# Kernel optimization log

Measured on AMD Instinct MI355X. Metric: run time of the kernel, lower is better.

Reference implementation:

```python
import jax, jax.numpy as jnp
import numpy as np
import math

N_EMBD = 1024
N_HEAD = 16
HEAD_DIM = N_EMBD // N_HEAD


def setup_inputs() -> dict:
    key = jax.random.key(0)
    ks = jax.random.split(key, 9)
    B, T, E = 4, 2048, N_EMBD
    s = 0.02
    inp = {
        "x": jax.random.normal(ks[0], (B, T, E), dtype=jnp.float32),
        "Wq": jax.random.normal(ks[1], (E, E), dtype=jnp.float32) * s,
        "bq": jnp.zeros((E,), dtype=jnp.float32),
        "Wk": jax.random.normal(ks[2], (E, E), dtype=jnp.float32) * s,
        "bk": jnp.zeros((E,), dtype=jnp.float32),
        "Wv": jax.random.normal(ks[3], (E, E), dtype=jnp.float32) * s,
        "bv": jnp.zeros((E,), dtype=jnp.float32),
        "Wo": jax.random.normal(ks[4], (E, E), dtype=jnp.float32) * s,
        "bo": jnp.zeros((E,), dtype=jnp.float32),
    }
    return inp


def reference(x, Wq, bq, Wk, bk, Wv, bv, Wo, bo):
    B, T, E = x.shape
    H, D = N_HEAD, HEAD_DIM
    # Linear projections (torch Linear: y = x @ W.T + b)
    Q = (x @ Wq.T + bq).reshape(B, T, H, D).transpose(0, 2, 1, 3)  # [B,H,T,D]
    K = (x @ Wk.T + bk).reshape(B, T, H, D).transpose(0, 2, 1, 3)
    V = (x @ Wv.T + bv).reshape(B, T, H, D).transpose(0, 2, 1, 3)
    scale = 1.0 / math.sqrt(D)
    scores = jnp.einsum("bhqd,bhkd->bhqk", Q, K) * scale  # [B,H,T,T]
    causal = jnp.tril(jnp.ones((T, T), dtype=bool))
    scores = jnp.where(causal, scores, jnp.float32(-jnp.inf))
    probs = jax.nn.softmax(scores, axis=-1)
    out = jnp.einsum("bhqk,bhkd->bhqd", probs, V)  # [B,H,T,D]
    out = out.transpose(0, 2, 1, 3).reshape(B, T, E)
    return out @ Wo.T + bo
```

## Files before the change

### kernel.cpp

```cpp
#include <hip/hip_runtime.h>
#include <math.h>


typedef __bf16 bf16x8 __attribute__((ext_vector_type(8)));
typedef float f32x4 __attribute__((ext_vector_type(4)));
typedef unsigned int u32x4 __attribute__((ext_vector_type(4)));
typedef unsigned int uint;
typedef unsigned short ushort;

#define B_ 4
#define T_ 2048
#define E_ 1024
#define H_ 16
#define D_ 64
#define BT_ (B_ * T_)

__device__ __forceinline__ f32x4 mfma16(bf16x8 a, bf16x8 b, f32x4 c) {
  return __builtin_amdgcn_mfma_f32_16x16x32_bf16(a, b, c, 0, 0, 0);
}

__device__ __forceinline__ void gl_lds16(void* lds, const void* g) {
  __builtin_amdgcn_global_load_lds(
      (__attribute__((address_space(1))) unsigned int*)g,
      (__attribute__((address_space(3))) unsigned int*)lds, 16, 0, 0);
}

__device__ __forceinline__ uint pkbf(float a, float b) {
  ushort ux = __builtin_bit_cast(ushort, (__bf16)a);
  ushort uy = __builtin_bit_cast(ushort, (__bf16)b);
  return (uint)ux | ((uint)uy << 16);
}

__global__ __launch_bounds__(256) void cvt_bf16(const float* __restrict__ in,
                                                __bf16* __restrict__ out, int n) {
  int i = (blockIdx.x * 256 + threadIdx.x) * 8;
  if (i >= n) return;
  float4 a = *(const float4*)&in[i];
  float4 b = *(const float4*)&in[i + 4];
  bf16x8 o;
  o[0] = (__bf16)a.x; o[1] = (__bf16)a.y; o[2] = (__bf16)a.z; o[3] = (__bf16)a.w;
  o[4] = (__bf16)b.x; o[5] = (__bf16)b.y; o[6] = (__bf16)b.z; o[7] = (__bf16)b.w;
  *(bf16x8*)&out[i] = o;
}

__global__ __launch_bounds__(256) void cvt_w4(const float* __restrict__ w0,
                                              const float* __restrict__ w1,
                                              const float* __restrict__ w2,
                                              const float* __restrict__ w3,
                                              __bf16* __restrict__ o0,
                                              __bf16* __restrict__ o1,
                                              __bf16* __restrict__ o2,
                                              __bf16* __restrict__ o3) {
  const float* in;
  __bf16* out;
  switch (blockIdx.y) {
    case 0: in = w0; out = o0; break;
    case 1: in = w1; out = o1; break;
    case 2: in = w2; out = o2; break;
    default: in = w3; out = o3; break;
  }
  int i = (blockIdx.x * 256 + threadIdx.x) * 8;
  float4 a = *(const float4*)&in[i];
  float4 b = *(const float4*)&in[i + 4];
  bf16x8 o;
  o[0] = (__bf16)a.x; o[1] = (__bf16)a.y; o[2] = (__bf16)a.z; o[3] = (__bf16)a.w;
  o[4] = (__bf16)b.x; o[5] = (__bf16)b.y; o[6] = (__bf16)b.z; o[7] = (__bf16)b.w;
  *(bf16x8*)&out[i] = o;
}

template <int MODE>
__global__ __launch_bounds__(256) void gemm_nt(const __bf16* __restrict__ A,
                                               const __bf16* __restrict__ Bm,
                                               const float* __restrict__ bias,
                                               void* __restrict__ out,
                                               int M, int N, int K) {
  __shared__ __bf16 sA[128 * 32];
  __shared__ __bf16 sB[128 * 32];
  const int tid = threadIdx.x;
  const int lane = tid & 63;
  const int wv = tid >> 6;
  const int wr = (wv >> 1) << 6;
  const int wc = (wv & 1) << 6;
  const int fr = lane & 15;
  const int fo = (lane >> 4) << 3;
  const int g = lane >> 4;
  const int m0 = blockIdx.y * 128;
  const int n0 = blockIdx.x * 128;

  f32x4 acc[4][4] = {};

  const __bf16* aRow = A + (size_t)(m0 + (tid >> 2)) * K + ((tid & 3) << 3);
  const __bf16* bRow = Bm + (size_t)(n0 + (tid >> 2)) * K + ((tid & 3) << 3);

  for (int kt = 0; kt < K; kt += 32) {
    gl_lds16(&sA[(size_t)tid * 8], aRow + kt);
    gl_lds16(&sA[(size_t)(256 + tid) * 8], aRow + (size_t)64 * K + kt);
    gl_lds16(&sB[(size_t)tid * 8], bRow + kt);
    gl_lds16(&sB[(size_t)(256 + tid) * 8], bRow + (size_t)64 * K + kt);
    __syncthreads();
    bf16x8 af[4], bq[4];
#pragma unroll
    for (int i = 0; i < 4; i++) af[i] = *(const bf16x8*)&sA[(wr + i * 16 + fr) * 32 + fo];
#pragma unroll
    for (int i = 0; i < 4; i++) bq[i] = *(const bf16x8*)&sB[(wc + i * 16 + fr) * 32 + fo];
#pragma unroll
    for (int i = 0; i < 4; i++)
#pragma unroll
      for (int j = 0; j < 4; j++) acc[i][j] = mfma16(af[i], bq[j], acc[i][j]);
    __syncthreads();
  }

#pragma unroll
  for (int i = 0; i < 4; i++) {
#pragma unroll
    for (int j = 0; j < 4; j++) {
#pragma unroll
      for (int r = 0; r < 4; r++) {
        const int m = m0 + wr + i * 16 + g * 4 + r;
        const int n = n0 + wc + j * 16 + fr;
        float v = acc[i][j][r] + bias[n];
        ((float*)out)[(size_t)m * N + n] = v;
      }
    }
  }
}

__global__ __launch_bounds__(256) void gemm_qkv(const __bf16* __restrict__ xb,
                                                const __bf16* __restrict__ Wq,
                                                const __bf16* __restrict__ Wk,
                                                const __bf16* __restrict__ Wv,
                                                const float* __restrict__ bq,
                                                const float* __restrict__ bk,
                                                const float* __restrict__ bv,
                                                __bf16* __restrict__ Qb,
                                                __bf16* __restrict__ Kb,
                                                __bf16* __restrict__ Vtb) {
  __shared__ __bf16 sA[128 * 32];
  __shared__ __bf16 sB[128 * 32];
  const int z = blockIdx.z;
  const __bf16* A;
  const __bf16* Bm;
  const float* bias;
  int m0, n0;
  if (z == 0) {
    A = xb; Bm = Wq; bias = bq;
    m0 = blockIdx.y * 128; n0 = blockIdx.x * 128;
  } else if (z == 1) {
    A = xb; Bm = Wk; bias = bk;
    m0 = blockIdx.y * 128; n0 = blockIdx.x * 128;
  } else {
    A = Wv; Bm = xb; bias = bv;
    m0 = blockIdx.x * 128; n0 = blockIdx.y * 128;
  }
  const int K = E_;
  const int tid = threadIdx.x;
  const int lane = tid & 63;
  const int wv = tid >> 6;
  const int wr = (wv >> 1) << 6;
  const int wc = (wv & 1) << 6;
  const int fr = lane & 15;
  const int fo = (lane >> 4) << 3;
  const int g = lane >> 4;

  f32x4 acc[4][4] = {};

  const __bf16* aRow = A + (size_t)(m0 + (tid >> 2)) * K + ((tid & 3) << 3);
  const __bf16* bRow = Bm + (size_t)(n0 + (tid >> 2)) * K + ((tid & 3) << 3);

  for (int kt = 0; kt < K; kt += 32) {
    gl_lds16(&sA[(size_t)tid * 8], aRow + kt);
    gl_lds16(&sA[(size_t)(256 + tid) * 8], aRow + (size_t)64 * K + kt);
    gl_lds16(&sB[(size_t)tid * 8], bRow + kt);
    gl_lds16(&sB[(size_t)(256 + tid) * 8], bRow + (size_t)64 * K + kt);
    __syncthreads();
    bf16x8 af[4], bq4[4];
#pragma unroll
    for (int i = 0; i < 4; i++) af[i] = *(const bf16x8*)&sA[(wr + i * 16 + fr) * 32 + fo];
#pragma unroll
    for (int i = 0; i < 4; i++) bq4[i] = *(const bf16x8*)&sB[(wc + i * 16 + fr) * 32 + fo];
#pragma unroll
    for (int i = 0; i < 4; i++)
#pragma unroll
      for (int j = 0; j < 4; j++) acc[i][j] = mfma16(af[i], bq4[j], acc[i][j]);
    __syncthreads();
  }

#pragma unroll
  for (int i = 0; i < 4; i++) {
#pragma unroll
    for (int j = 0; j < 4; j++) {
#pragma unroll
      for (int r = 0; r < 4; r++) {
        const int m = m0 + wr + i * 16 + g * 4 + r;
        const int n = n0 + wc + j * 16 + fr;
        float v = acc[i][j][r];
        if (z == 2) {
          v += bias[m];
          const int b = n >> 11, t = n & (T_ - 1);
          const int h = m >> 6, d = m & 63;
          Vtb[(((size_t)b * H_ + h) * D_ + d) * T_ + t] = (__bf16)v;
        } else {
          v += bias[n];
          const int b = m >> 11, t = m & (T_ - 1);
          const int h = n >> 6, d = n & 63;
          __bf16* out = (z == 0) ? Qb : Kb;
          out[(((size_t)b * H_ + h) * T_ + t) * D_ + d] = (__bf16)v;
        }
      }
    }
  }
}

__global__ __launch_bounds__(512) void attn_fwd(const __bf16* __restrict__ Q,
                                                const __bf16* __restrict__ Kg,
                                                const __bf16* __restrict__ Vt,
                                                __bf16* __restrict__ O) {
  __shared__ __bf16 sK[2][64 * 64];
  __shared__ __bf16 sV[2][64 * 64];
  const int tid = threadIdx.x;
  const int lane = tid & 63;
  const int wv = tid >> 6;
  const int fr = lane & 15;
  const int g = lane >> 4;
  const int k = blockIdx.x;
  const int bh = (k & 7) | ((k >> 6) << 3);
  const int pr = (k >> 3) & 7;
  const __bf16* Qp = Q + (size_t)bh * T_ * D_;
  const __bf16* Kp = Kg + (size_t)bh * T_ * D_;
  const __bf16* Vp = Vt + (size_t)bh * D_ * T_;
  const float SCL = 0.125f * 1.44269504088896f;
  const int addrA = (fr + 32 * (g & 1)) * 4;
  const int swz = fr & 7;
  const int b = bh >> 4, h = bh & 15;

  auto stage = [&](int buf, int kv0) {
    const int row = tid >> 3, ch = tid & 7;
    gl_lds16(&sK[buf][tid * 8],
             Kp + (size_t)(kv0 + row) * D_ + ((ch ^ (row & 7)) << 3));
    gl_lds16(&sV[buf][tid * 8],
             Vp + (size_t)row * T_ + kv0 + ((ch ^ (row & 7)) << 3));
  };

#pragma unroll 1
  for (int pass = 0; pass < 2; ++pass) {
    const int s = pass ? 15 - pr : pr;
    const int qw = s * 128 + wv * 16;
    const int ntile = 2 * s + 2;

    bf16x8 qf[2];
#pragma unroll
    for (int kc = 0; kc < 2; kc++)
      qf[kc] = *(const bf16x8*)&Qp[(size_t)(qw + fr) * D_ + kc * 32 + g * 8];

    f32x4 acc[4] = {};
    float mrun = -INFINITY;
    float lrun = 0.f;

    stage(0, 0);
    __syncthreads();
    int cur = 0;

#pragma unroll 1
    for (int kt = 0; kt < ntile; ++kt) {
      const int kv0 = kt << 6;
      if (kt + 1 < ntile) stage(cur ^ 1, (kt + 1) << 6);

      if (kv0 <= qw + 15) {
        f32x4 st[4] = {};
        __builtin_amdgcn_s_setprio(1);
#pragma unroll
        for (int kvf = 0; kvf < 4; ++kvf) {
          const int row = kvf * 16 + fr;
          bf16x8 kf0 = *(const bf16x8*)&sK[cur][row * 64 + ((g ^ swz) << 3)];
          bf16x8 kf1 = *(const bf16x8*)&sK[cur][row * 64 + (((g + 4) ^ swz) << 3)];
          st[kvf] = mfma16(kf0, qf[0], st[kvf]);
          st[kvf] = mfma16(kf1, qf[1], st[kvf]);
        }
        __builtin_amdgcn_s_setprio(0);

        if (kv0 + 63 > qw) {
#pragma unroll
          for (int kvf = 0; kvf < 4; ++kvf)
#pragma unroll
            for (int r = 0; r < 4; ++r)
              if (kv0 + kvf * 16 + g * 4 + r > qw + fr) st[kvf][r] = -INFINITY;
        }

        float rm[4];
#pragma unroll
        for (int kvf = 0; kvf < 4; ++kvf)
          rm[kvf] = fmaxf(fmaxf(st[kvf][0], st[kvf][1]),
                          fmaxf(st[kvf][2], st[kvf][3]));
        float rmax = fmaxf(fmaxf(rm[0], rm[1]), fmaxf(rm[2], rm[3])) * SCL;

        if (!__all(rmax - mrun <= 8.f)) {
          float rfull = fmaxf(rmax, __shfl_xor(rmax, 16, 64));
          rfull = fmaxf(rfull, __shfl_xor(rfull, 32, 64));
          const float mn = fmaxf(mrun, rfull);
          const float corr = exp2f(mrun - mn);
          mrun = mn;
          lrun *= corr;
          float cg[4];
#pragma unroll
          for (int r = 0; r < 4; ++r) cg[r] = __shfl(corr, g * 4 + r, 64);
#pragma unroll
          for (int nd = 0; nd < 4; ++nd)
#pragma unroll
            for (int r = 0; r < 4; ++r) acc[nd][r] *= cg[r];
        }

        float p[4][4];
        float ls = 0.f;
#pragma unroll
        for (int kvf = 0; kvf < 4; ++kvf)
#pragma unroll
          for (int r = 0; r < 4; ++r) {
            p[kvf][r] = exp2f(fmaf(st[kvf][r], SCL, -mrun));
            ls += p[kvf][r];
          }
        lrun += ls;

        uint w[4][2];
#pragma unroll
        for (int kvf = 0; kvf < 4; ++kvf) {
          w[kvf][0] = pkbf(p[kvf][0], p[kvf][1]);
          w[kvf][1] = pkbf(p[kvf][2], p[kvf][3]);
        }
        uint W[2][4];
#pragma unroll
        for (int kc = 0; kc < 2; ++kc)
#pragma unroll
          for (int m = 0; m < 4; ++m) {
            const int a = addrA + (m >> 1) * 64;
            int t0 = __builtin_amdgcn_ds_bpermute(a, (int)w[2 * kc][m & 1]);
            int t1 = __builtin_amdgcn_ds_bpermute(a, (int)w[2 * kc + 1][m & 1]);
            W[kc][m] = (uint)((g >> 1) ? t1 : t0);
          }

        __builtin_amdgcn_s_setprio(1);
#pragma unroll
        for (int kc = 0; kc < 2; ++kc) {
          u32x4 t;
          t[0] = W[kc][0]; t[1] = W[kc][1]; t[2] = W[kc][2]; t[3] = W[kc][3];
          bf16x8 pa = __builtin_bit_cast(bf16x8, t);
#pragma unroll
          for (int nd = 0; nd < 4; ++nd) {
            const int row = nd * 16 + fr;
            bf16x8 vf =
                *(const bf16x8*)&sV[cur][row * 64 + (((4 * kc + g) ^ swz) << 3)];
            acc[nd] = mfma16(pa, vf, acc[nd]);
          }
        }
        __builtin_amdgcn_s_setprio(0);
      }

      __syncthreads();
      cur ^= 1;
    }

    lrun += __shfl_xor(lrun, 16, 64);
    lrun += __shfl_xor(lrun, 32, 64);
    float linv[4];
#pragma unroll
    for (int r = 0; r < 4; ++r) linv[r] = 1.f / __shfl(lrun, g * 4 + r, 64);
#pragma unroll
    for (int nd = 0; nd < 4; ++nd)
#pragma unroll
      for (int r = 0; r < 4; ++r) {
        const int t = qw + g * 4 + r;
        O[(((size_t)b * T_ + t) * H_ + h) * D_ + nd * 16 + fr] =
            (__bf16)(acc[nd][r] * linv[r]);
      }
  }
}

extern "C" void kernel_launch(void* const* d_in, const int* in_sizes, int n_in,
                              void* d_out, int out_size, void* d_ws, size_t ws_size,
                              hipStream_t stream) {
  const float* x  = (const float*)d_in[0];
  const float* Wq = (const float*)d_in[1];
  const float* bq = (const float*)d_in[2];
  const float* Wk = (const float*)d_in[3];
  const float* bk = (const float*)d_in[4];
  const float* Wv = (const float*)d_in[5];
  const float* bv = (const float*)d_in[6];
  const float* Wo = (const float*)d_in[7];
  const float* bo = (const float*)d_in[8];

  char* w = (char*)d_ws;
  __bf16* xb  = (__bf16*)w; w += (size_t)BT_ * E_ * 2;
  __bf16* Wqb = (__bf16*)w; w += (size_t)E_ * E_ * 2;
  __bf16* Wkb = (__bf16*)w; w += (size_t)E_ * E_ * 2;
  __bf16* Wvb = (__bf16*)w; w += (size_t)E_ * E_ * 2;
  __bf16* Wob = (__bf16*)w; w += (size_t)E_ * E_ * 2;
  __bf16* Qb  = (__bf16*)w; w += (size_t)BT_ * E_ * 2;
  __bf16* Kb  = (__bf16*)w; w += (size_t)BT_ * E_ * 2;
  __bf16* Vtb = (__bf16*)w; w += (size_t)BT_ * E_ * 2;
  __bf16* Ob  = (__bf16*)w; w += (size_t)BT_ * E_ * 2;

  cvt_bf16<<<(BT_ * E_) / 2048, 256, 0, stream>>>(x, xb, BT_ * E_);
  cvt_w4<<<dim3((E_ * E_) / 2048, 4), 256, 0, stream>>>(Wq, Wk, Wv, Wo,
                                                        Wqb, Wkb, Wvb, Wob);

  gemm_qkv<<<dim3(E_ / 128, BT_ / 128, 3), 256, 0, stream>>>(
      xb, Wqb, Wkb, Wvb, bq, bk, bv, Qb, Kb, Vtb);

  attn_fwd<<<512, 512, 0, stream>>>(Qb, Kb, Vtb, Ob);

  gemm_nt<2><<<dim3(E_ / 128, BT_ / 128), 256, 0, stream>>>(Ob, Wob, bo, d_out, BT_, E_, E_);
}
```

Measured before the change: 207.9 us.

## Use 128-wide KV tiles in attention, fold softmax scale into Q, swap grid order

The attention kernel now stages 128-key K/V tiles instead of 64, with a wider XOR swizzle for V. This halves the number of tile iterations and barriers per query block, at the cost of doubled LDS and more registers for the score and probability arrays. The softmax scale times log2(e) is folded into Q in the QKV GEMM epilogue, which removes a multiply per score. The QKV and output GEMM grids are swapped so blockIdx.x walks the M dimension, which changes the block launch order and L2 reuse.

```diff
diff --git a/kernel.cpp b/kernel.cpp
--- a/kernel.cpp
+++ b/kernel.cpp
@@ -30,6 +30,8 @@
   ushort uy = __builtin_bit_cast(ushort, (__bf16)b);
   return (uint)ux | ((uint)uy << 16);
 }
+
+#define QSCL 0.18033688011112f
 
 __global__ __launch_bounds__(256) void cvt_bf16(const float* __restrict__ in,
                                                 __bf16* __restrict__ out, int n) {
@@ -68,12 +70,11 @@
   *(bf16x8*)&out[i] = o;
 }
 
-template <int MODE>
-__global__ __launch_bounds__(256) void gemm_nt(const __bf16* __restrict__ A,
-                                               const __bf16* __restrict__ Bm,
-                                               const float* __restrict__ bias,
-                                               void* __restrict__ out,
-                                               int M, int N, int K) {
+__global__ __launch_bounds__(256) void gemm_out(const __bf16* __restrict__ A,
+                                                const __bf16* __restrict__ Bm,
+                                                const float* __restrict__ bias,
+                                                float* __restrict__ out,
+                                                int M, int N, int K) {
   __shared__ __bf16 sA[128 * 32];
   __shared__ __bf16 sB[128 * 32];
   const int tid = threadIdx.x;
@@ -84,8 +85,8 @@
   const int fr = lane & 15;
   const int fo = (lane >> 4) << 3;
   const int g = lane >> 4;
-  const int m0 = blockIdx.y * 128;
-  const int n0 = blockIdx.x * 128;
+  const int m0 = blockIdx.x * 128;
+  const int n0 = blockIdx.y * 128;
 
   f32x4 acc[4][4] = {};
 
@@ -118,8 +119,7 @@
       for (int r = 0; r < 4; r++) {
         const int m = m0 + wr + i * 16 + g * 4 + r;
         const int n = n0 + wc + j * 16 + fr;
-        float v = acc[i][j][r] + bias[n];
-        ((float*)out)[(size_t)m * N + n] = v;
+        out[(size_t)m * N + n] = acc[i][j][r] + bias[n];
       }
     }
   }
@@ -144,13 +144,13 @@
   int m0, n0;
   if (z == 0) {
     A = xb; Bm = Wq; bias = bq;
-    m0 = blockIdx.y * 128; n0 = blockIdx.x * 128;
+    m0 = blockIdx.x * 128; n0 = blockIdx.y * 128;
   } else if (z == 1) {
     A = xb; Bm = Wk; bias = bk;
-    m0 = blockIdx.y * 128; n0 = blockIdx.x * 128;
+    m0 = blockIdx.x * 128; n0 = blockIdx.y * 128;
   } else {
     A = Wv; Bm = xb; bias = bv;
-    m0 = blockIdx.x * 128; n0 = blockIdx.y * 128;
+    m0 = blockIdx.y * 128; n0 = blockIdx.x * 128;
   }
   const int K = E_;
   const int tid = threadIdx.x;
@@ -201,6 +201,7 @@
           Vtb[(((size_t)b * H_ + h) * D_ + d) * T_ + t] = (__bf16)v;
         } else {
           v += bias[n];
+          if (z == 0) v *= QSCL;
           const int b = m >> 11, t = m & (T_ - 1);
           const int h = n >> 6, d = n & 63;
           __bf16* out = (z == 0) ? Qb : Kb;
@@ -215,8 +216,8 @@
                                                 const __bf16* __restrict__ Kg,
                                                 const __bf16* __restrict__ Vt,
                                                 __bf16* __restrict__ O) {
-  __shared__ __bf16 sK[2][64 * 64];
-  __shared__ __bf16 sV[2][64 * 64];
+  __shared__ __bf16 sK[2][128 * 64];
+  __shared__ __bf16 sV[2][64 * 128];
   const int tid = threadIdx.x;
   const int lane = tid & 63;
   const int wv = tid >> 6;
@@ -228,24 +229,27 @@
   const __bf16* Qp = Q + (size_t)bh * T_ * D_;
   const __bf16* Kp = Kg + (size_t)bh * T_ * D_;
   const __bf16* Vp = Vt + (size_t)bh * D_ * T_;
-  const float SCL = 0.125f * 1.44269504088896f;
   const int addrA = (fr + 32 * (g & 1)) * 4;
-  const int swz = fr & 7;
   const int b = bh >> 4, h = bh & 15;
 
   auto stage = [&](int buf, int kv0) {
-    const int row = tid >> 3, ch = tid & 7;
-    gl_lds16(&sK[buf][tid * 8],
-             Kp + (size_t)(kv0 + row) * D_ + ((ch ^ (row & 7)) << 3));
-    gl_lds16(&sV[buf][tid * 8],
-             Vp + (size_t)row * T_ + kv0 + ((ch ^ (row & 7)) << 3));
+#pragma unroll
+    for (int rr = 0; rr < 2; ++rr) {
+      const int idx = rr * 512 + tid;
+      const int krow = idx >> 3, kch = idx & 7;
+      gl_lds16(&sK[buf][idx * 8],
+               Kp + (size_t)(kv0 + krow) * D_ + ((kch ^ (krow & 7)) << 3));
+      const int vrow = idx >> 4, vch = idx & 15;
+      gl_lds16(&sV[buf][idx * 8],
+               Vp + (size_t)vrow * T_ + kv0 + ((vch ^ (vrow & 15)) << 3));
+    }
   };
 
 #pragma unroll 1
   for (int pass = 0; pass < 2; ++pass) {
     const int s = pass ? 15 - pr : pr;
     const int qw = s * 128 + wv * 16;
-    const int ntile = 2 * s + 2;
+    const int ntile = s + 1;
 
     bf16x8 qf[2];
 #pragma unroll
@@ -262,97 +266,97 @@
 
 #pragma unroll 1
     for (int kt = 0; kt < ntile; ++kt) {
-      const int kv0 = kt << 6;
-      if (kt + 1 < ntile) stage(cur ^ 1, (kt + 1) << 6);
-
-      if (kv0 <= qw + 15) {
-        f32x4 st[4] = {};
-        __builtin_amdgcn_s_setprio(1);
-#pragma unroll
-        for (int kvf = 0; kvf < 4; ++kvf) {
-          const int row = kvf * 16 + fr;
-          bf16x8 kf0 = *(const bf16x8*)&sK[cur][row * 64 + ((g ^ swz) << 3)];
-          bf16x8 kf1 = *(const bf16x8*)&sK[cur][row * 64 + (((g + 4) ^ swz) << 3)];
-          st[kvf] = mfma16(kf0, qf[0], st[kvf]);
-          st[kvf] = mfma16(kf1, qf[1], st[kvf]);
+      const int kv0 = kt << 7;
+      if (kt + 1 < ntile) stage(cur ^ 1, (kt + 1) << 7);
+
+      f32x4 st[8] = {};
+      __builtin_amdgcn_s_setprio(1);
+#pragma unroll
+      for (int kvf = 0; kvf < 8; ++kvf) {
+        const int row = kvf * 16 + fr;
+        bf16x8 kf0 = *(const bf16x8*)&sK[cur][row * 64 + ((g ^ (fr & 7)) << 3)];
+        bf16x8 kf1 =
+            *(const bf16x8*)&sK[cur][row * 64 + (((g + 4) ^ (fr & 7)) << 3)];
+        st[kvf] = mfma16(kf0, qf[0], st[kvf]);
+        st[kvf] = mfma16(kf1, qf[1], st[kvf]);
+      }
+      __builtin_amdgcn_s_setprio(0);
+
+      if (kv0 + 127 > qw) {
+#pragma unroll
+        for (int kvf = 0; kvf < 8; ++kvf)
+#pragma unroll
+          for (int r = 0; r < 4; ++r)
+            if (kv0 + kvf * 16 + g * 4 + r > qw + fr) st[kvf][r] = -INFINITY;
+      }
+
+      float rm[8];
+#pragma unroll
+      for (int kvf = 0; kvf < 8; ++kvf)
+        rm[kvf] =
+            fmaxf(fmaxf(st[kvf][0], st[kvf][1]), fmaxf(st[kvf][2], st[kvf][3]));
+      float rmax = fmaxf(fmaxf(fmaxf(rm[0], rm[1]), fmaxf(rm[2], rm[3])),
+                         fmaxf(fmaxf(rm[4], rm[5]), fmaxf(rm[6], rm[7])));
+
+      if (!__all(rmax - mrun <= 8.f)) {
+        float rfull = fmaxf(rmax, __shfl_xor(rmax, 16, 64));
+        rfull = fmaxf(rfull, __shfl_xor(rfull, 32, 64));
+        const float mn = fmaxf(mrun, rfull);
+        const float corr = exp2f(mrun - mn);
+        mrun = mn;
+        lrun *= corr;
+        float cg[4];
+#pragma unroll
+        for (int r = 0; r < 4; ++r) cg[r] = __shfl(corr, g * 4 + r, 64);
+#pragma unroll
+        for (int nd = 0; nd < 4; ++nd)
+#pragma unroll
+          for (int r = 0; r < 4; ++r) acc[nd][r] *= cg[r];
+      }
+
+      float p[8][4];
+      float ls = 0.f;
+#pragma unroll
+      for (int kvf = 0; kvf < 8; ++kvf)
+#pragma unroll
+        for (int r = 0; r < 4; ++r) {
+          p[kvf][r] = exp2f(st[kvf][r] - mrun);
+          ls += p[kvf][r];
         }
-        __builtin_amdgcn_s_setprio(0);
-
-        if (kv0 + 63 > qw) {
-#pragma unroll
-          for (int kvf = 0; kvf < 4; ++kvf)
-#pragma unroll
-            for (int r = 0; r < 4; ++r)
-              if (kv0 + kvf * 16 + g * 4 + r > qw + fr) st[kvf][r] = -INFINITY;
+      lrun += ls;
+
+      uint w[8][2];
+#pragma unroll
+      for (int kvf = 0; kvf < 8; ++kvf) {
+        w[kvf][0] = pkbf(p[kvf][0], p[kvf][1]);
+        w[kvf][1] = pkbf(p[kvf][2], p[kvf][3]);
+      }
+      uint W[4][4];
+#pragma unroll
+      for (int kc = 0; kc < 4; ++kc)
+#pragma unroll
+        for (int m = 0; m < 4; ++m) {
+          const int a = addrA + (m >> 1) * 64;
+          int t0 = __builtin_amdgcn_ds_bpermute(a, (int)w[2 * kc][m & 1]);
+          int t1 = __builtin_amdgcn_ds_bpermute(a, (int)w[2 * kc + 1][m & 1]);
+          W[kc][m] = (uint)((g >> 1) ? t1 : t0);
         }
 
-        float rm[4];
-#pragma unroll
-        for (int kvf = 0; kvf < 4; ++kvf)
-          rm[kvf] = fmaxf(fmaxf(st[kvf][0], st[kvf][1]),
-                          fmaxf(st[kvf][2], st[kvf][3]));
-        float rmax = fmaxf(fmaxf(rm[0], rm[1]), fmaxf(rm[2], rm[3])) * SCL;
-
-        if (!__all(rmax - mrun <= 8.f)) {
-          float rfull = fmaxf(rmax, __shfl_xor(rmax, 16, 64));
-          rfull = fmaxf(rfull, __shfl_xor(rfull, 32, 64));
-          const float mn = fmaxf(mrun, rfull);
-          const float corr = exp2f(mrun - mn);
-          mrun = mn;
-          lrun *= corr;
-          float cg[4];
-#pragma unroll
-          for (int r = 0; r < 4; ++r) cg[r] = __shfl(corr, g * 4 + r, 64);
-#pragma unroll
-          for (int nd = 0; nd < 4; ++nd)
-#pragma unroll
-            for (int r = 0; r < 4; ++r) acc[nd][r] *= cg[r];
+      __builtin_amdgcn_s_setprio(1);
+#pragma unroll
+      for (int kc = 0; kc < 4; ++kc) {
+        u32x4 t;
+        t[0] = W[kc][0]; t[1] = W[kc][1]; t[2] = W[kc][2]; t[3] = W[kc][3];
+        bf16x8 pa = __builtin_bit_cast(bf16x8, t);
+#pragma unroll
+        for (int nd = 0; nd < 4; ++nd) {
+          const int row = nd * 16 + fr;
+          bf16x8 vf =
+              *(const bf16x8*)&sV[cur][row * 128 + (((4 * kc + g) ^ fr) << 3)];
+          acc[nd] = mfma16(pa, vf, acc[nd]);
         }
-
-        float p[4][4];
-        float ls = 0.f;
-#pragma unroll
-        for (int kvf = 0; kvf < 4; ++kvf)
-#pragma unroll
-          for (int r = 0; r < 4; ++r) {
-            p[kvf][r] = exp2f(fmaf(st[kvf][r], SCL, -mrun));
-            ls += p[kvf][r];
-          }
-        lrun += ls;
-
-        uint w[4][2];
-#pragma unroll
-        for (int kvf = 0; kvf < 4; ++kvf) {
-          w[kvf][0] = pkbf(p[kvf][0], p[kvf][1]);
-          w[kvf][1] = pkbf(p[kvf][2], p[kvf][3]);
-        }
-        uint W[2][4];
-#pragma unroll
-        for (int kc = 0; kc < 2; ++kc)
-#pragma unroll
-          for (int m = 0; m < 4; ++m) {
-            const int a = addrA + (m >> 1) * 64;
-            int t0 = __builtin_amdgcn_ds_bpermute(a, (int)w[2 * kc][m & 1]);
-            int t1 = __builtin_amdgcn_ds_bpermute(a, (int)w[2 * kc + 1][m & 1]);
-            W[kc][m] = (uint)((g >> 1) ? t1 : t0);
-          }
-
-        __builtin_amdgcn_s_setprio(1);
-#pragma unroll
-        for (int kc = 0; kc < 2; ++kc) {
-          u32x4 t;
-          t[0] = W[kc][0]; t[1] = W[kc][1]; t[2] = W[kc][2]; t[3] = W[kc][3];
-          bf16x8 pa = __builtin_bit_cast(bf16x8, t);
-#pragma unroll
-          for (int nd = 0; nd < 4; ++nd) {
-            const int row = nd * 16 + fr;
-            bf16x8 vf =
-                *(const bf16x8*)&sV[cur][row * 64 + (((4 * kc + g) ^ swz) << 3)];
-            acc[nd] = mfma16(pa, vf, acc[nd]);
-          }
-        }
-        __builtin_amdgcn_s_setprio(0);
-      }
+      }
+      __builtin_amdgcn_s_setprio(0);
 
       __syncthreads();
       cur ^= 1;
@@ -402,10 +406,11 @@
   cvt_w4<<<dim3((E_ * E_) / 2048, 4), 256, 0, stream>>>(Wq, Wk, Wv, Wo,
                                                         Wqb, Wkb, Wvb, Wob);
 
-  gemm_qkv<<<dim3(E_ / 128, BT_ / 128, 3), 256, 0, stream>>>(
+  gemm_qkv<<<dim3(BT_ / 128, E_ / 128, 3), 256, 0, stream>>>(
       xb, Wqb, Wkb, Wvb, bq, bk, bv, Qb, Kb, Vtb);
 
   attn_fwd<<<512, 512, 0, stream>>>(Qb, Kb, Vtb, Ob);
 
-  gemm_nt<2><<<dim3(E_ / 128, BT_ / 128), 256, 0, stream>>>(Ob, Wob, bo, d_out, BT_, E_, E_);
-}
+  gemm_out<<<dim3(BT_ / 128, E_ / 128), 256, 0, stream>>>(
+      Ob, Wob, bo, (float*)d_out, BT_, E_, E_);
+}
```

New measurement: 202.1 us. 2.8% less time.
